# Optimization experiments

Measured on AMD Instinct MI355X. Metric: run time of the kernel, lower is better.

## Reference

```python
import jax, jax.numpy as jnp
import numpy as np

PATCH, STRIDE, TOPK, EPS = 16, 8, 8, 1e-8

def _leaky(x):
    return jax.nn.leaky_relu(x, 0.01)

def setup_inputs() -> dict:
    key = jax.random.key(0)
    ks = jax.random.split(key, 12)
    s = 0.05  # small weight scale to avoid tanh saturation
    return {
        "X":      jax.random.normal(ks[0], (16, 4096, 512), jnp.float32),
        "W_enc1": jax.random.normal(ks[1], (512, 256), jnp.float32) * s,
        "b_enc1": jax.random.normal(ks[2], (256,), jnp.float32) * s,
        "W_enc2": jax.random.normal(ks[3], (256, 64), jnp.float32) * s,
        "b_enc2": jax.random.normal(ks[4], (64,), jnp.float32) * s,
        "Wq":     jax.random.normal(ks[5], (64, 64), jnp.float32) * s,
        "Wk":     jax.random.normal(ks[6], (64, 64), jnp.float32) * s,
        "Wv":     jax.random.normal(ks[7], (64, 64), jnp.float32) * s,
        "W_agg":  jax.random.normal(ks[8], (64, 64), jnp.float32) * s,
        "b_agg":  jax.random.normal(ks[9], (64,), jnp.float32) * s,
        "W_dec":  jax.random.normal(ks[10], (64, 512), jnp.float32) * s,
        "b_dec":  jax.random.normal(ks[11], (512,), jnp.float32) * s,
    }

def reference(X, W_enc1, b_enc1, W_enc2, b_enc2, Wq, Wk, Wv, W_agg, b_agg, W_dec, b_dec):
    B, L, D = X.shape
    # var_encoder (dropout-free MLP)
    Xe = _leaky(X @ W_enc1 + b_enc1) @ W_enc2 + b_enc2          # (B, L, d)
    d = Xe.shape[-1]
    # unfold into overlapping patches
    h = (L - PATCH) // STRIDE + 1
    pos = jnp.arange(h)[:, None] * STRIDE + jnp.arange(PATCH)[None, :]  # (h, PATCH)
    patches = Xe[:, pos, :]                                      # (B, h, PATCH, d)
    per_patch = patches.mean(axis=2).reshape(B * h, d)           # (N, d)
    q = per_patch @ Wq
    k = per_patch @ Wk
    v = per_patch @ Wv                                           # (N, hqk)
    qn = q / (jnp.linalg.norm(q, axis=-1, keepdims=True) + EPS)
    kn = k / (jnp.linalg.norm(k, axis=-1, keepdims=True) + EPS)
    # antisymmetric outer product, (N, hqk, hqk)
    M = qn[:, :, None] * kn[:, None, :] - kn[:, :, None] * qn[:, None, :]
    A = jax.nn.relu(jnp.tanh(M))
    n = A.shape[-1]
    # topk pruning along last dim via scatter-style mask
    _, idx = jax.lax.top_k(A, TOPK)                              # (N, n, TOPK)
    mask = jnp.any(idx[..., None] == jnp.arange(n), axis=-2)     # (N, n, n) bool
    A = A * mask.astype(A.dtype)
    A = A / jnp.maximum(A.sum(axis=-1, keepdims=True), EPS)
    Av = jnp.einsum('nij,nj->ni', A, v)                          # (N, hqk)
    # after_agg (dropout = identity in eval)
    z = _leaky(Av @ W_agg + b_agg)                               # (N, d)
    zB = z.reshape(B, h, d)
    # overlap-add fold: each patch writes its (constant-over-time) z to its window
    seg = jnp.broadcast_to(zB[:, :, None, :], (B, h, PATCH, d)).reshape(B, h * PATCH, d)
    flat_pos = pos.reshape(-1)                                   # (h*PATCH,)
    out = jnp.zeros((B, L, d), X.dtype).at[:, flat_pos, :].add(seg)
    counts = jnp.zeros((L,), X.dtype).at[flat_pos].add(1.0)
    out = out / jnp.maximum(counts, 1.0)[None, :, None]
    return out @ W_dec + b_dec                                   # (B, L, D)
```

## Files before the change

### kernel.cpp

```cpp
#include <hip/hip_runtime.h>


typedef __attribute__((ext_vector_type(8))) _Float16 half8;
typedef __attribute__((ext_vector_type(4))) _Float16 half4;
typedef __attribute__((ext_vector_type(4))) float floatx4;

__device__ __forceinline__ _Float16 f2h(float f) { return (_Float16)f; }

#define MFMA16(A, B, C) __builtin_amdgcn_mfma_f32_16x16x32_f16((A), (B), (C), 0, 0, 0)

__global__ __launch_bounds__(256) void prep_weights(
    const float* __restrict__ W1, const float* __restrict__ W2,
    const float* __restrict__ Wd,
    _Float16* __restrict__ W1t, _Float16* __restrict__ W2t,
    _Float16* __restrict__ Wdt)
{
    int idx = blockIdx.x * 256 + threadIdx.x;
    { int n = idx >> 9, k = idx & 511;  W1t[idx] = f2h(W1[k * 256 + n]); }
    if (idx < 16384) { int n = idx >> 8, k = idx & 255; W2t[idx] = f2h(W2[k * 64 + n]); }
    if (idx < 32768) { int n = idx >> 6, k = idx & 63;  Wdt[idx] = f2h(Wd[k * 512 + n]); }
}

__global__ __launch_bounds__(256) void enc_fused(
    const float* __restrict__ X, const _Float16* __restrict__ W1t,
    const float* __restrict__ b1, const _Float16* __restrict__ W2t,
    const float* __restrict__ b2, float* __restrict__ Xe)
{
    __shared__ _Float16 smem[21504];
    _Float16* As  = smem;
    _Float16* Bs  = smem + 4608;
    _Float16* Hs  = smem;
    _Float16* W2s = smem + 16896;

    const int tid  = threadIdx.x;
    const int lane = tid & 63;
    const int w    = tid >> 6;
    const int m0   = blockIdx.x * 64;

    const int arow  = tid >> 2;
    const int akseg = (tid & 3) << 4;
    const float* Abase = X + (size_t)(m0 + arow) * 512 + akseg;

    const int brow0  = (w << 6) + (lane >> 3);
    const int bchunk = (((lane & 7) ^ ((lane >> 3) & 7)) << 3);

    floatx4 acc1[4][4];
#pragma unroll
    for (int ci = 0; ci < 4; ci++)
#pragma unroll
        for (int mi = 0; mi < 4; mi++) acc1[ci][mi] = (floatx4){0.f, 0.f, 0.f, 0.f};

    float4 pa[4];
    auto loadA = [&](int kt) {
#pragma unroll
        for (int u = 0; u < 4; u++) pa[u] = *(const float4*)(Abase + kt + 4 * u);
    };

    loadA(0);
    for (int kt = 0; kt < 512; kt += 64) {
#pragma unroll
        for (int inst = 0; inst < 8; inst++) {
            const _Float16* src = W1t + (size_t)(brow0 + inst * 8) * 512 + kt + bchunk;
            __builtin_amdgcn_global_load_lds(
                (const __attribute__((address_space(1))) unsigned int*)src,
                (__attribute__((address_space(3))) unsigned int*)(Bs + ((w << 6) + inst * 8) * 64),
                16, 0, 0);
        }
        {
            _Float16* d = &As[arow * 72 + akseg];
#pragma unroll
            for (int h = 0; h < 2; h++) {
                float4 f0 = pa[2 * h], f1 = pa[2 * h + 1];
                half8 o;
                o[0] = f2h(f0.x); o[1] = f2h(f0.y); o[2] = f2h(f0.z); o[3] = f2h(f0.w);
                o[4] = f2h(f1.x); o[5] = f2h(f1.y); o[6] = f2h(f1.z); o[7] = f2h(f1.w);
                *(half8*)(d + 8 * h) = o;
            }
        }
        __syncthreads();
        if (kt + 64 < 512) loadA(kt + 64);
#pragma unroll
        for (int ks = 0; ks < 2; ks++) {
            const int lchunk = ks * 4 + (lane >> 4);
            half8 af[4], bf[4];
#pragma unroll
            for (int ci = 0; ci < 4; ci++) {
                const int c = (w << 6) + ci * 16 + (lane & 15);
                af[ci] = *(const half8*)&Bs[c * 64 + ((lchunk ^ (lane & 7)) << 3)];
            }
#pragma unroll
            for (int mi = 0; mi < 4; mi++)
                bf[mi] = *(const half8*)&As[(mi * 16 + (lane & 15)) * 72 + ks * 32 + ((lane >> 4) << 3)];
#pragma unroll
            for (int ci = 0; ci < 4; ci++)
#pragma unroll
                for (int mi = 0; mi < 4; mi++)
                    acc1[ci][mi] = MFMA16(af[ci], bf[mi], acc1[ci][mi]);
        }
        __syncthreads();
    }

    float4 b1v[4];
#pragma unroll
    for (int ci = 0; ci < 4; ci++)
        b1v[ci] = *(const float4*)&b1[(w << 6) + ci * 16 + ((lane >> 4) << 2)];
#pragma unroll
    for (int ci = 0; ci < 4; ci++) {
        const int cb = (w << 6) + ci * 16 + ((lane >> 4) << 2);
#pragma unroll
        for (int mi = 0; mi < 4; mi++) {
            const int m = mi * 16 + (lane & 15);
            half4 hv;
#pragma unroll
            for (int r = 0; r < 4; r++) {
                float v = acc1[ci][mi][r] + ((const float*)&b1v[ci])[r];
                v = v > 0.f ? v : 0.01f * v;
                hv[r] = f2h(v);
            }
            *(half4*)&Hs[m * 264 + cb] = hv;
        }
    }

    floatx4 acc2[4];
#pragma unroll
    for (int ni = 0; ni < 4; ni++) acc2[ni] = (floatx4){0.f, 0.f, 0.f, 0.f};
    const int w2n   = tid >> 2;
    const int w2seg = (tid & 3) << 4;
#pragma unroll
    for (int p = 0; p < 4; p++) {
        *(half8*)&W2s[w2n * 72 + w2seg]     = *(const half8*)&W2t[w2n * 256 + p * 64 + w2seg];
        *(half8*)&W2s[w2n * 72 + w2seg + 8] = *(const half8*)&W2t[w2n * 256 + p * 64 + w2seg + 8];
        __syncthreads();
#pragma unroll
        for (int ks = 0; ks < 2; ks++) {
            half8 a2 = *(const half8*)&Hs[((w << 4) + (lane & 15)) * 264 + p * 64 + ks * 32 + ((lane >> 4) << 3)];
            half8 b2f[4];
#pragma unroll
            for (int ni = 0; ni < 4; ni++)
                b2f[ni] = *(const half8*)&W2s[(ni * 16 + (lane & 15)) * 72 + ks * 32 + ((lane >> 4) << 3)];
#pragma unroll
            for (int ni = 0; ni < 4; ni++)
                acc2[ni] = MFMA16(a2, b2f[ni], acc2[ni]);
        }
        __syncthreads();
    }
#pragma unroll
    for (int ni = 0; ni < 4; ni++) {
        const float bb = b2[ni * 16 + (lane & 15)];
#pragma unroll
        for (int r = 0; r < 4; r++) {
            const int row = m0 + (w << 4) + ((lane >> 4) << 2) + r;
            Xe[(size_t)row * 64 + ni * 16 + (lane & 15)] = acc2[ni][r] + bb;
        }
    }
}

#define TOP8_INS(mv) do { float _x = (mv); float _t;            \
    _t = fmaxf(s0,_x); _x = fminf(s0,_x); s0 = _t;              \
    _t = fmaxf(s1,_x); _x = fminf(s1,_x); s1 = _t;              \
    _t = fmaxf(s2,_x); _x = fminf(s2,_x); s2 = _t;              \
    _t = fmaxf(s3,_x); _x = fminf(s3,_x); s3 = _t;              \
    _t = fmaxf(s4,_x); _x = fminf(s4,_x); s4 = _t;              \
    _t = fmaxf(s5,_x); _x = fminf(s5,_x); s5 = _t;              \
    _t = fmaxf(s6,_x); _x = fminf(s6,_x); s6 = _t;              \
    s7 = fmaxf(s7,_x); } while (0)

__global__ __launch_bounds__(256) void patch_attn(
    const float* __restrict__ Xe,  const float* __restrict__ Wq,
    const float* __restrict__ Wk,  const float* __restrict__ Wv,
    const float* __restrict__ Wagg, const float* __restrict__ bagg,
    float* __restrict__ zout)
{
    __shared__ float sh[4][336];
    const int w    = threadIdx.x >> 6;
    const int lane = threadIdx.x & 63;
    const int n = blockIdx.x * 4 + w;
    const int b = n / 511;
    const int i = n - b * 511;
    float* pp  = &sh[w][0];
    float* qs  = pp + 64;
    float* ksm = pp + 128;
    float* vsm = pp + 192;
    float* avs = pp + 256;

    const float* xb = Xe + ((size_t)(b * 4096 + i * 8)) * 64 + lane;
    float s = 0.f;
#pragma unroll
    for (int p = 0; p < 16; p++) s += xb[(size_t)p * 64];
    pp[lane] = s * 0.0625f;
    __syncthreads();

    float q = 0.f, k = 0.f, v = 0.f;
#pragma unroll 4
    for (int e = 0; e < 64; e += 4) {
        float4 p4 = *(const float4*)&pp[e];
        q = fmaf(p4.x, Wq[(e+0)*64+lane], q); q = fmaf(p4.y, Wq[(e+1)*64+lane], q);
        q = fmaf(p4.z, Wq[(e+2)*64+lane], q); q = fmaf(p4.w, Wq[(e+3)*64+lane], q);
        k = fmaf(p4.x, Wk[(e+0)*64+lane], k); k = fmaf(p4.y, Wk[(e+1)*64+lane], k);
        k = fmaf(p4.z, Wk[(e+2)*64+lane], k); k = fmaf(p4.w, Wk[(e+3)*64+lane], k);
        v = fmaf(p4.x, Wv[(e+0)*64+lane], v); v = fmaf(p4.y, Wv[(e+1)*64+lane], v);
        v = fmaf(p4.z, Wv[(e+2)*64+lane], v); v = fmaf(p4.w, Wv[(e+3)*64+lane], v);
    }
    float sq = q * q, sk = k * k;
#pragma unroll
    for (int o = 1; o < 64; o <<= 1) { sq += __shfl_xor(sq, o); sk += __shfl_xor(sk, o); }
    const float qni = q / (sqrtf(sq) + 1e-8f);
    const float kni = k / (sqrtf(sk) + 1e-8f);
    qs[lane] = qni; ksm[lane] = kni; vsm[lane] = v;
    __syncthreads();

    auto MV = [&](float kj, float qj) { return fmaf(qni, kj, -(kni * qj)); };

    float s0=-1e30f,s1=-1e30f,s2=-1e30f,s3=-1e30f,s4=-1e30f,s5=-1e30f,s6=-1e30f,s7=-1e30f;
#pragma unroll
    for (int j = 0; j < 64; j += 4) {
        float4 k4 = *(const float4*)&ksm[j];
        float4 q4 = *(const float4*)&qs[j];
        TOP8_INS(MV(k4.x, q4.x)); TOP8_INS(MV(k4.y, q4.y));
        TOP8_INS(MV(k4.z, q4.z)); TOP8_INS(MV(k4.w, q4.w));
    }
    const float teff = fmaxf(s7, 1e-37f) * (1.f - 1.2e-7f);

    float ssum = 0.f, av = 0.f;
#pragma unroll
    for (int j = 0; j < 64; j += 4) {
        float4 k4 = *(const float4*)&ksm[j];
        float4 q4 = *(const float4*)&qs[j];
        float4 v4 = *(const float4*)&vsm[j];
#define P2(KJ, QJ, VJ) do { float _m = MV(KJ, QJ); float _x2 = _m * _m;           \
        float _a = _m * (15.f + _x2) * __builtin_amdgcn_rcpf(fmaf(6.f, _x2, 15.f)); \
        float _am = (_m >= teff) ? _a : 0.f;                                       \
        ssum += _am; av = fmaf(_am, (VJ), av); } while (0)
        P2(k4.x, q4.x, v4.x); P2(k4.y, q4.y, v4.y);
        P2(k4.z, q4.z, v4.z); P2(k4.w, q4.w, v4.w);
#undef P2
    }
    avs[lane] = av / fmaxf(ssum, 1e-8f);
    __syncthreads();

    float zc = bagg[lane];
#pragma unroll 4
    for (int e = 0; e < 64; e += 4) {
        float4 a4 = *(const float4*)&avs[e];
        zc = fmaf(a4.x, Wagg[(e+0)*64+lane], zc); zc = fmaf(a4.y, Wagg[(e+1)*64+lane], zc);
        zc = fmaf(a4.z, Wagg[(e+2)*64+lane], zc); zc = fmaf(a4.w, Wagg[(e+3)*64+lane], zc);
    }
    zc = zc > 0.f ? zc : 0.01f * zc;
    zout[(size_t)n * 64 + lane] = zc;
}

__global__ __launch_bounds__(256) void dec_fused(
    const float* __restrict__ z, const _Float16* __restrict__ Wdt,
    const float* __restrict__ bd, float* __restrict__ out)
{
    __shared__ _Float16 As[128 * 72];
    __shared__ _Float16 Bs[128 * 72];
    const int tid  = threadIdx.x;
    const int lane = tid & 63;
    const int w    = tid >> 6;
    const int m0 = blockIdx.y * 128, n0 = blockIdx.x * 128;
    const int wrow = (w & 1) << 6, wcol = (w >> 1) << 6;

    {
        const int arow  = tid >> 1;
        const int akseg = (tid & 1) << 5;
        const int row = m0 + arow;
        const int b = row >> 12, l = row & 4095, g = l >> 3;
        const int g0 = g - 1 >= 0 ? g - 1 : 0;
        const int g1 = g <= 510 ? g : 510;
        const float w0 = (g >= 1) ? 1.f : 0.f;
        const float w1 = (g <= 510) ? 1.f : 0.f;
        const float sc = (w0 + w1) > 1.5f ? 0.5f : 1.f;
        const float* z0 = z + ((size_t)(b * 511 + g0)) * 64 + akseg;
        const float* z1 = z + ((size_t)(b * 511 + g1)) * 64 + akseg;
        _Float16* d = &As[arow * 72 + akseg];
#pragma unroll
        for (int u = 0; u < 4; u++) {
            float4 f0a = *(const float4*)(z0 + 8 * u);
            float4 f0b = *(const float4*)(z0 + 8 * u + 4);
            float4 f1a = *(const float4*)(z1 + 8 * u);
            float4 f1b = *(const float4*)(z1 + 8 * u + 4);
            half8 o;
            o[0] = f2h((f0a.x * w0 + f1a.x * w1) * sc);
            o[1] = f2h((f0a.y * w0 + f1a.y * w1) * sc);
            o[2] = f2h((f0a.z * w0 + f1a.z * w1) * sc);
            o[3] = f2h((f0a.w * w0 + f1a.w * w1) * sc);
            o[4] = f2h((f0b.x * w0 + f1b.x * w1) * sc);
            o[5] = f2h((f0b.y * w0 + f1b.y * w1) * sc);
            o[6] = f2h((f0b.z * w0 + f1b.z * w1) * sc);
            o[7] = f2h((f0b.w * w0 + f1b.w * w1) * sc);
            *(half8*)(d + 8 * u) = o;
        }
    }
    {
        const int brow  = tid >> 1;
        const int bkseg = (tid & 1) << 5;
        const _Float16* s = Wdt + (size_t)(n0 + brow) * 64 + bkseg;
        _Float16* d = &Bs[brow * 72 + bkseg];
#pragma unroll
        for (int u = 0; u < 4; u++) *(half8*)(d + 8 * u) = *(const half8*)(s + 8 * u);
    }
    __syncthreads();

    floatx4 acc[2][4];
    floatx4 accf[4][4];
#pragma unroll
    for (int mi = 0; mi < 4; mi++)
#pragma unroll
        for (int ni = 0; ni < 4; ni++) accf[mi][ni] = (floatx4){0.f, 0.f, 0.f, 0.f};
    (void)acc;
#pragma unroll
    for (int ks = 0; ks < 2; ks++) {
        const int koff = ks * 32 + ((lane >> 4) << 3);
        half8 af[4], bf[4];
#pragma unroll
        for (int mi = 0; mi < 4; mi++)
            af[mi] = *(const half8*)&As[(wrow + mi * 16 + (lane & 15)) * 72 + koff];
#pragma unroll
        for (int ni = 0; ni < 4; ni++)
            bf[ni] = *(const half8*)&Bs[(wcol + ni * 16 + (lane & 15)) * 72 + koff];
#pragma unroll
        for (int mi = 0; mi < 4; mi++)
#pragma unroll
            for (int ni = 0; ni < 4; ni++)
                accf[mi][ni] = MFMA16(af[mi], bf[ni], accf[mi][ni]);
    }

    float bvv[4];
#pragma unroll
    for (int ni = 0; ni < 4; ni++) bvv[ni] = bd[n0 + wcol + ni * 16 + (lane & 15)];

    float* Cs = (float*)As;
#pragma unroll
    for (int c = 0; c < 4; c++) {
        __syncthreads();
        const int own_wrow = ((c * 32) / 64) * 64;
        if (wrow == own_wrow) {
#pragma unroll
            for (int mm = 0; mm < 2; mm++) {
                const int mi = ((c * 32) % 64) / 16 + mm;
#pragma unroll
                for (int ni = 0; ni < 4; ni++) {
#pragma unroll
                    for (int r = 0; r < 4; r++) {
                        const int lr  = mm * 16 + ((lane >> 4) << 2) + r;
                        const int col = wcol + ni * 16 + (lane & 15);
                        Cs[lr * 128 + col] = accf[mi][ni][r] + bvv[ni];
                    }
                }
            }
        }
        __syncthreads();
#pragma unroll
        for (int u = 0; u < 4; u++) {
            const int idx = (u * 256 + tid) * 4;
            const int lr = idx >> 7, col = idx & 127;
            float4 vv = *(const float4*)&Cs[idx];
            *(float4*)&out[(size_t)(m0 + c * 32 + lr) * 512 + n0 + col] = vv;
        }
    }
}

extern "C" void kernel_launch(void* const* d_in, const int* in_sizes, int n_in,
                              void* d_out, int out_size, void* d_ws, size_t ws_size,
                              hipStream_t stream)
{
    const float* X    = (const float*)d_in[0];
    const float* W1   = (const float*)d_in[1];
    const float* b1   = (const float*)d_in[2];
    const float* W2   = (const float*)d_in[3];
    const float* b2   = (const float*)d_in[4];
    const float* Wq   = (const float*)d_in[5];
    const float* Wk   = (const float*)d_in[6];
    const float* Wv   = (const float*)d_in[7];
    const float* Wagg = (const float*)d_in[8];
    const float* bagg = (const float*)d_in[9];
    const float* Wd   = (const float*)d_in[10];
    const float* bd   = (const float*)d_in[11];

    char* ws = (char*)d_ws;
    float*    Xe  = (float*)(ws);
    float*    z   = (float*)(ws + 16777216);
    _Float16* W1t = (_Float16*)(ws + 18870272);
    _Float16* W2t = (_Float16*)(ws + 19132416);
    _Float16* Wdt = (_Float16*)(ws + 19165184);
    float* out = (float*)d_out;

    prep_weights<<<512, 256, 0, stream>>>(W1, W2, Wd, W1t, W2t, Wdt);
    enc_fused<<<1024, 256, 0, stream>>>(X, W1t, b1, W2t, b2, Xe);
    patch_attn<<<2044, 256, 0, stream>>>(Xe, Wq, Wk, Wv, Wagg, bagg, z);
    dec_fused<<<dim3(4, 512), 256, 0, stream>>>(z, Wdt, bd, out);
}
```

Baseline: 318.3 us.

## Sum hidden rows per 8-row group before second encoder GEMM, emit group sums

The patch mean is linear in the encoder's second layer, so the activated hidden rows are summed over aligned groups of 8 (via lane shuffles) before multiplying by W2. The kernel now writes one 64-wide group sum per 8 rows (with 8x bias) instead of the full per-row Xe. patch_attn then forms each patch mean from two adjacent group sums rather than reading 16 rows. This cuts the second GEMM's work by 8x, shrinks the intermediate buffer and the global traffic between the two kernels, and drops the shared-memory staging of W2. In exchange it adds cross-lane reductions and a final fp16 rounding of the summed hidden values, which changes numerics slightly.

```diff
diff --git a/kernel.cpp b/kernel.cpp
--- a/kernel.cpp
+++ b/kernel.cpp
@@ -24,13 +24,12 @@
 __global__ __launch_bounds__(256) void enc_fused(
     const float* __restrict__ X, const _Float16* __restrict__ W1t,
     const float* __restrict__ b1, const _Float16* __restrict__ W2t,
-    const float* __restrict__ b2, float* __restrict__ Xe)
-{
-    __shared__ _Float16 smem[21504];
-    _Float16* As  = smem;
-    _Float16* Bs  = smem + 4608;
-    _Float16* Hs  = smem;
-    _Float16* W2s = smem + 16896;
+    const float* __restrict__ b2, float* __restrict__ Gs)
+{
+    __shared__ _Float16 smem[20992];
+    _Float16* As   = smem;
+    _Float16* Bs   = smem + 4608;
+    _Float16* Hs16 = smem;
 
     const int tid  = threadIdx.x;
     const int lane = tid & 63;
@@ -106,51 +105,47 @@
         b1v[ci] = *(const float4*)&b1[(w << 6) + ci * 16 + ((lane >> 4) << 2)];
 #pragma unroll
     for (int ci = 0; ci < 4; ci++) {
-        const int cb = (w << 6) + ci * 16 + ((lane >> 4) << 2);
 #pragma unroll
         for (int mi = 0; mi < 4; mi++) {
-            const int m = mi * 16 + (lane & 15);
-            half4 hv;
+            float vs[4];
 #pragma unroll
             for (int r = 0; r < 4; r++) {
                 float v = acc1[ci][mi][r] + ((const float*)&b1v[ci])[r];
-                v = v > 0.f ? v : 0.01f * v;
-                hv[r] = f2h(v);
-            }
-            *(half4*)&Hs[m * 264 + cb] = hv;
-        }
-    }
-
-    floatx4 acc2[4];
-#pragma unroll
-    for (int ni = 0; ni < 4; ni++) acc2[ni] = (floatx4){0.f, 0.f, 0.f, 0.f};
-    const int w2n   = tid >> 2;
-    const int w2seg = (tid & 3) << 4;
-#pragma unroll
-    for (int p = 0; p < 4; p++) {
-        *(half8*)&W2s[w2n * 72 + w2seg]     = *(const half8*)&W2t[w2n * 256 + p * 64 + w2seg];
-        *(half8*)&W2s[w2n * 72 + w2seg + 8] = *(const half8*)&W2t[w2n * 256 + p * 64 + w2seg + 8];
-        __syncthreads();
-#pragma unroll
-        for (int ks = 0; ks < 2; ks++) {
-            half8 a2 = *(const half8*)&Hs[((w << 4) + (lane & 15)) * 264 + p * 64 + ks * 32 + ((lane >> 4) << 3)];
-            half8 b2f[4];
-#pragma unroll
-            for (int ni = 0; ni < 4; ni++)
-                b2f[ni] = *(const half8*)&W2s[(ni * 16 + (lane & 15)) * 72 + ks * 32 + ((lane >> 4) << 3)];
-#pragma unroll
-            for (int ni = 0; ni < 4; ni++)
-                acc2[ni] = MFMA16(a2, b2f[ni], acc2[ni]);
-        }
-        __syncthreads();
-    }
-#pragma unroll
-    for (int ni = 0; ni < 4; ni++) {
-        const float bb = b2[ni * 16 + (lane & 15)];
+                vs[r] = v > 0.f ? v : 0.01f * v;
+            }
+#pragma unroll
+            for (int r = 0; r < 4; r++) {
+                vs[r] += __shfl_xor(vs[r], 1);
+                vs[r] += __shfl_xor(vs[r], 2);
+                vs[r] += __shfl_xor(vs[r], 4);
+            }
+            if ((lane & 7) == 0) {
+                const int gl = 2 * mi + ((lane & 15) >> 3);
+                half4 hv;
+#pragma unroll
+                for (int r = 0; r < 4; r++) hv[r] = f2h(vs[r]);
+                *(half4*)&Hs16[gl * 264 + (w << 6) + ci * 16 + ((lane >> 4) << 2)] = hv;
+            }
+        }
+    }
+    __syncthreads();
+
+    floatx4 acc2 = (floatx4){0.f, 0.f, 0.f, 0.f};
+    const int kq = (lane >> 4) << 3;
+#pragma unroll
+    for (int ks = 0; ks < 8; ks++) {
+        half8 af = *(const half8*)&Hs16[(lane & 15) * 264 + ks * 32 + kq];
+        half8 bf = *(const half8*)&W2t[(size_t)((w << 4) + (lane & 15)) * 256 + ks * 32 + kq];
+        acc2 = MFMA16(af, bf, acc2);
+    }
+    if (lane < 32) {
+        const int n = (w << 4) + (lane & 15);
+        const float bb = 8.f * b2[n];
+        const int gbase = blockIdx.x * 8;
 #pragma unroll
         for (int r = 0; r < 4; r++) {
-            const int row = m0 + (w << 4) + ((lane >> 4) << 2) + r;
-            Xe[(size_t)row * 64 + ni * 16 + (lane & 15)] = acc2[ni][r] + bb;
+            const int g = ((lane >> 4) << 2) + r;
+            Gs[(size_t)(gbase + g) * 64 + n] = acc2[r] + bb;
         }
     }
 }
@@ -166,7 +161,7 @@
     s7 = fmaxf(s7,_x); } while (0)
 
 __global__ __launch_bounds__(256) void patch_attn(
-    const float* __restrict__ Xe,  const float* __restrict__ Wq,
+    const float* __restrict__ Gs,  const float* __restrict__ Wq,
     const float* __restrict__ Wk,  const float* __restrict__ Wv,
     const float* __restrict__ Wagg, const float* __restrict__ bagg,
     float* __restrict__ zout)
@@ -183,11 +178,8 @@
     float* vsm = pp + 192;
     float* avs = pp + 256;
 
-    const float* xb = Xe + ((size_t)(b * 4096 + i * 8)) * 64 + lane;
-    float s = 0.f;
-#pragma unroll
-    for (int p = 0; p < 16; p++) s += xb[(size_t)p * 64];
-    pp[lane] = s * 0.0625f;
+    const float* gp = Gs + ((size_t)(b * 512 + i)) * 64 + lane;
+    pp[lane] = (gp[0] + gp[64]) * 0.0625f;
     __syncthreads();
 
     float q = 0.f, k = 0.f, v = 0.f;
@@ -302,13 +294,11 @@
     }
     __syncthreads();
 
-    floatx4 acc[2][4];
     floatx4 accf[4][4];
 #pragma unroll
     for (int mi = 0; mi < 4; mi++)
 #pragma unroll
         for (int ni = 0; ni < 4; ni++) accf[mi][ni] = (floatx4){0.f, 0.f, 0.f, 0.f};
-    (void)acc;
 #pragma unroll
     for (int ks = 0; ks < 2; ks++) {
         const int koff = ks * 32 + ((lane >> 4) << 3);
@@ -379,15 +369,15 @@
     const float* bd   = (const float*)d_in[11];
 
     char* ws = (char*)d_ws;
-    float*    Xe  = (float*)(ws);
-    float*    z   = (float*)(ws + 16777216);
-    _Float16* W1t = (_Float16*)(ws + 18870272);
-    _Float16* W2t = (_Float16*)(ws + 19132416);
-    _Float16* Wdt = (_Float16*)(ws + 19165184);
+    float*    Gs  = (float*)(ws);
+    float*    z   = (float*)(ws + 2097152);
+    _Float16* W1t = (_Float16*)(ws + 4194304);
+    _Float16* W2t = (_Float16*)(ws + 4456448);
+    _Float16* Wdt = (_Float16*)(ws + 4489216);
     float* out = (float*)d_out;
 
     prep_weights<<<512, 256, 0, stream>>>(W1, W2, Wd, W1t, W2t, Wdt);
-    enc_fused<<<1024, 256, 0, stream>>>(X, W1t, b1, W2t, b2, Xe);
-    patch_attn<<<2044, 256, 0, stream>>>(Xe, Wq, Wk, Wv, Wagg, bagg, z);
+    enc_fused<<<1024, 256, 0, stream>>>(X, W1t, b1, W2t, b2, Gs);
+    patch_attn<<<2044, 256, 0, stream>>>(Gs, Wq, Wk, Wv, Wagg, bagg, z);
     dec_fused<<<dim3(4, 512), 256, 0, stream>>>(z, Wdt, bd, out);
 }
```

Result: no change. 317.4 us (-0.3%).
